# Performance work log

Hardware: AMD Instinct MI355X
Metric: run time of the kernel (lower is better)

Reference implementation:

```python
import jax, jax.numpy as jnp
import numpy as np

N_AGENT = 25
N_S = 32
N_A = 4
HID = 128
EHH_HID = HID * N_AGENT          # 3200
INTER = 150                      # INTERMEDIATE_NODES
BATCH = 2048
N_EDGE = 300


def _leaky(x):
    return jnp.where(x >= 0, x, 0.01 * x)


def setup_inputs() -> dict:
    key = jax.random.key(0)
    ks = jax.random.split(key, 12)
    states = jax.random.normal(ks[0], (N_AGENT, BATCH, N_S), dtype=jnp.float32)
    ehh_w = jax.random.normal(ks[1], (N_AGENT * N_S, EHH_HID), dtype=jnp.float32) * 0.05
    anova = jax.random.normal(ks[2], (EHH_HID + INTER, N_AGENT), dtype=jnp.float32)
    w1 = jax.random.normal(ks[3], (N_AGENT, EHH_HID, 12), dtype=jnp.float32) * 0.02
    b1 = jax.random.normal(ks[4], (N_AGENT, 12), dtype=jnp.float32) * 0.02
    w2 = jax.random.normal(ks[5], (N_AGENT, 12, 12), dtype=jnp.float32) * 0.3
    b2 = jax.random.normal(ks[6], (N_AGENT, 12), dtype=jnp.float32) * 0.02
    w3 = jax.random.normal(ks[7], (N_AGENT, 12, N_A), dtype=jnp.float32) * 0.3
    b3 = jax.random.normal(ks[8], (N_AGENT, N_A), dtype=jnp.float32) * 0.02
    actions = jax.random.randint(ks[9], (N_AGENT, BATCH), 0, N_A, dtype=jnp.int32)
    # adjacency rows: (bi_att_row, neighbor_row_a, unused, neighbor_row_b)
    c0 = jax.random.randint(ks[10], (N_EDGE, 1), 0, INTER, dtype=jnp.int32)
    c13 = jax.random.randint(ks[11], (N_EDGE, 2), 0, EHH_HID, dtype=jnp.int32)
    adj = jnp.concatenate([c0, c13[:, :1], jnp.zeros((N_EDGE, 1), jnp.int32), c13[:, 1:]], axis=1)
    return {"states": states, "ehh_w": ehh_w, "anova": anova,
            "w1": w1, "b1": b1, "w2": w2, "b2": b2, "w3": w3, "b3": b3,
            "actions": actions, "adj": adj}


def reference(states, ehh_w, anova, w1, b1, w2, b2, w3, b3, actions, adj):
    # states: (A, B, S) -> ehh_s: (B, A*S)   (torch.cat(states, dim=1))
    B = states.shape[1]
    ehh_s = jnp.transpose(states, (1, 0, 2)).reshape(B, -1)
    # EHH normalization (BatchNorm, affine=False, batch stats) + linear + LeakyReLU
    mu = jnp.mean(ehh_s, axis=0, keepdims=True)
    var = jnp.var(ehh_s, axis=0, keepdims=True)
    ehh_n = (ehh_s - mu) * jax.lax.rsqrt(var + 1e-5)
    ehh_embedding = _leaky(ehh_n @ ehh_w)                    # (B, EHH_HID)

    # ANOVA attention assembly via adjacency scatter
    self_att = anova[:EHH_HID, :]                            # (EHH_HID, A)
    bi_att = anova[EHH_HID:, :]                              # (INTER, A)
    vals = bi_att[adj[:, 0], :]                              # (E, A)
    neighbor_att = jnp.zeros((EHH_HID, N_AGENT), jnp.float32)
    neighbor_att = neighbor_att.at[adj[:, 1]].set(vals)
    neighbor_att = neighbor_att.at[adj[:, 3]].set(vals)
    all_att = (self_att + neighbor_att).T                    # (A, EHH_HID)

    # att_s repeat/permute/reshape == broadcast of embedding per agent
    att_out = ehh_embedding[:, None, :] * all_att[None, :, :]  # (B, A, EHH_HID)

    # per-agent critics (ehh_hidden -> 12 -> 12 -> n_a)
    h1 = _leaky(jnp.einsum('bah,ahk->bak', att_out, w1) + b1[None])
    h2 = _leaky(jnp.einsum('bak,akj->baj', h1, w2) + b2[None])
    all_q = jnp.einsum('baj,ajc->bac', h2, w3) + b3[None]     # (B, A, N_A)

    # q = all_q.gather(1, in_acs) per agent -> (A, B)
    q = jnp.take_along_axis(all_q, actions.T[:, :, None], axis=2)[..., 0].T
    return q
```

## Files before the change

kernel.cpp:

```cpp
#include <hip/hip_runtime.h>
#include <cstdint>

#define NAG 25
#define NS 32
#define EHH 3200
#define KDIM 800
#define BATCH 2048
#define NEDGE 300
#define NPAD 384
#define KSPLIT 5

typedef _Float16 half8 __attribute__((ext_vector_type(8)));
typedef float f32x4 __attribute__((ext_vector_type(4)));

__device__ __forceinline__ float leaky(float x) { return x >= 0.f ? x : 0.01f * x; }

__global__ __launch_bounds__(256)
void prep1_kernel(const float* __restrict__ states, const float* __restrict__ ehh_w,
                  const int* __restrict__ adj, const float* __restrict__ anova,
                  const float* __restrict__ w1,
                  float* __restrict__ mean, float* __restrict__ rstd,
                  _Float16* __restrict__ wt, _Float16* __restrict__ w2dt) {
    __shared__ float redS[32][32];
    __shared__ float redQ[32][32];
    __shared__ float tile[32][33];
    __shared__ int win[EHH];
    const int bi = blockIdx.x;
    const int tid = threadIdx.x;

    if (bi < 25) {
        const int a = bi;
        const int s4 = (tid & 7) << 2;
        const int r0 = tid >> 3;
        const float* base = states + ((size_t)a * BATCH + r0) * NS + s4;
        f32x4 sum = {0.f, 0.f, 0.f, 0.f};
        f32x4 sq  = {0.f, 0.f, 0.f, 0.f};
#pragma unroll 8
        for (int it = 0; it < 64; ++it) {
            f32x4 v = *(const f32x4*)(base + (size_t)it * 32 * NS);
            sum += v;
            sq  += v * v;
        }
        *(f32x4*)&redS[r0][s4] = sum;
        *(f32x4*)&redQ[r0][s4] = sq;
        __syncthreads();
        if (tid < 32) {
            float s = 0.f, q = 0.f;
#pragma unroll
            for (int r = 0; r < 32; ++r) { s += redS[r][tid]; q += redQ[r][tid]; }
            float m = s * (1.f / BATCH);
            float var = q * (1.f / BATCH) - m * m;
            mean[a * 32 + tid] = m;
            rstd[a * 32 + tid] = rsqrtf(var + 1e-5f);
        }
    } else if (bi < 2525) {
        const int bb = bi - 25;
        const int n0 = (bb % 100) * 32, k0 = (bb / 100) * 32;
        const int x = tid & 31, y = tid >> 5;
        for (int i = y; i < 32; i += 8)
            tile[i][x] = ehh_w[(size_t)(k0 + i) * EHH + n0 + x];
        __syncthreads();
        for (int i = y; i < 32; i += 8)
            wt[(size_t)(n0 + i) * KDIM + k0 + x] = (_Float16)tile[x][i];
    } else {
        const int bb = bi - 2525;
        if (bb < 313) {
            for (int h = tid; h < EHH; h += 256) win[h] = -1;
            __syncthreads();
            for (int e = tid; e < 2 * NEDGE; e += 256) {
                int pass = e >= NEDGE;
                int ee = pass ? e - NEDGE : e;
                int dest = adj[ee * 4 + (pass ? 3 : 1)];
                atomicMax(&win[dest], e);
            }
            __syncthreads();
            int t = bb * 256 + tid;
            if (t < NAG * EHH) {
                int a = t / EHH;
                int h = t - a * EHH;
                float att = anova[(size_t)h * NAG + a];
                int w = win[h];
                if (w >= 0) {
                    int ee = w >= NEDGE ? w - NEDGE : w;
                    att += anova[(size_t)(EHH + adj[ee * 4]) * NAG + a];
                }
                const float* wp = w1 + ((size_t)a * EHH + h) * 12;
#pragma unroll
                for (int kk = 0; kk < 12; ++kk)
                    w2dt[(size_t)(a * 12 + kk) * EHH + h] = (_Float16)(att * wp[kk]);
            }
        } else {
            int p = (bb - 313) * 256 + tid;
            if (p < (NPAD - 300) * EHH / 8) {
                half8 z = {0, 0, 0, 0, 0, 0, 0, 0};
                ((half8*)(w2dt + (size_t)300 * EHH))[p] = z;
            }
        }
    }
}

__global__ __launch_bounds__(256)
void norm_kernel(const float* __restrict__ states, const float* __restrict__ mean,
                 const float* __restrict__ rstd, _Float16* __restrict__ A) {
    int u = blockIdx.x * 256 + threadIdx.x;
    int b = u / 100;
    int fo = (u - b * 100) * 8;
    int a = fo >> 5, s = fo & 31;
    const float* sp = states + ((size_t)a * BATCH + b) * NS + s;
    f32x4 v0 = *(const f32x4*)sp;
    f32x4 v1 = *(const f32x4*)(sp + 4);
    f32x4 m0 = *(const f32x4*)(mean + fo);
    f32x4 m1 = *(const f32x4*)(mean + fo + 4);
    f32x4 r0 = *(const f32x4*)(rstd + fo);
    f32x4 r1 = *(const f32x4*)(rstd + fo + 4);
    half8 out;
#pragma unroll
    for (int i = 0; i < 4; ++i) out[i] = (_Float16)((v0[i] - m0[i]) * r0[i]);
#pragma unroll
    for (int i = 0; i < 4; ++i) out[4 + i] = (_Float16)((v1[i] - m1[i]) * r1[i]);
    *(half8*)(A + (size_t)b * KDIM + fo) = out;
}

__device__ __forceinline__ void async16(const void* g, void* l) {
    __builtin_amdgcn_global_load_lds(
        (const __attribute__((address_space(1))) void*)(uintptr_t)g,
        (__attribute__((address_space(3))) void*)(unsigned)(uintptr_t)l, 16, 0, 0);
}

template <int MI, int NI, bool LEAKY_F16_OUT>
__global__ __launch_bounds__(256)
void gemm_bt(const _Float16* __restrict__ A, const _Float16* __restrict__ B,
             _Float16* __restrict__ Ch, float* __restrict__ Cf,
             int Ktot, int ldc, int kPerSplit, int slabStride) {
    constexpr int BM = MI * 32;
    constexpr int BN = NI * 32;
    __shared__ __attribute__((aligned(16))) _Float16 As[2][BM * 32];
    __shared__ __attribute__((aligned(16))) _Float16 Bs[2][BN * 32];
    const int tid = threadIdx.x;
    const int lane = tid & 63;
    const int wave = tid >> 6;
    const int wm = (wave >> 1) * (MI * 16);
    const int wn = (wave & 1) * (NI * 16);

    const int gx = gridDim.x, gy = gridDim.y;
    int nwg = gx * gy * gridDim.z;
    int bidf = blockIdx.x + gx * (blockIdx.y + gy * blockIdx.z);
    int swz = (bidf & 7) * (nwg >> 3) + (bidf >> 3);
    const int bx = swz % gx;
    const int rem = swz / gx;
    const int by = rem % gy;
    const int bz = rem / gy;

    const int m0 = bx * BM;
    const int n0 = by * BN;
    const int k0 = bz * kPerSplit;
    const int nk = kPerSplit >> 5;

    const int srow = lane >> 2;
    const int scol = (lane & 3) << 3;
    const _Float16* gA0 = A + (size_t)(m0 + wave * 16 + srow) * Ktot + k0 + scol;
    const _Float16* gA1 = gA0 + (size_t)64 * Ktot;
    const _Float16* gB0 = B + (size_t)(n0 + wave * 16 + srow) * Ktot + k0 + scol;
    const _Float16* gB1 = gB0 + (size_t)64 * Ktot;
    const int lofs = wave * 512;

    f32x4 acc[MI][NI];
    const f32x4 zero = {0.f, 0.f, 0.f, 0.f};
#pragma unroll
    for (int i = 0; i < MI; ++i)
#pragma unroll
        for (int j = 0; j < NI; ++j) acc[i][j] = zero;

    const int fr = lane & 15;
    const int q8 = (lane >> 4) << 3;

    async16(gA0, As[0] + lofs);
    if constexpr (BM == 128) async16(gA1, As[0] + 2048 + lofs);
    async16(gB0, Bs[0] + lofs);
    if constexpr (BN == 128) async16(gB1, Bs[0] + 2048 + lofs);

    for (int kt = 0; kt < nk; ++kt) {
        const int cur = kt & 1;
        __syncthreads();
        if (kt + 1 < nk) {
            const int ko = (kt + 1) << 5;
            const int nxt = cur ^ 1;
            async16(gA0 + ko, As[nxt] + lofs);
            if constexpr (BM == 128) async16(gA1 + ko, As[nxt] + 2048 + lofs);
            async16(gB0 + ko, Bs[nxt] + lofs);
            if constexpr (BN == 128) async16(gB1 + ko, Bs[nxt] + 2048 + lofs);
        }
        half8 av[MI], bv[NI];
#pragma unroll
        for (int i = 0; i < MI; ++i)
            av[i] = *(const half8*)(As[cur] + (wm + i * 16 + fr) * 32 + q8);
#pragma unroll
        for (int j = 0; j < NI; ++j)
            bv[j] = *(const half8*)(Bs[cur] + (wn + j * 16 + fr) * 32 + q8);
#pragma unroll
        for (int i = 0; i < MI; ++i)
#pragma unroll
            for (int j = 0; j < NI; ++j)
                acc[i][j] = __builtin_amdgcn_mfma_f32_16x16x32_f16(av[i], bv[j], acc[i][j], 0, 0, 0);
    }

    const int r0 = (lane >> 4) << 2;
    if (LEAKY_F16_OUT) {
#pragma unroll
        for (int i = 0; i < MI; ++i)
#pragma unroll
            for (int j = 0; j < NI; ++j)
#pragma unroll
                for (int r = 0; r < 4; ++r) {
                    int row = m0 + wm + i * 16 + r0 + r;
                    int col = n0 + wn + j * 16 + fr;
                    Ch[(size_t)row * ldc + col] = (_Float16)leaky(acc[i][j][r]);
                }
    } else {
        float* C = Cf + (size_t)bz * slabStride;
#pragma unroll
        for (int i = 0; i < MI; ++i)
#pragma unroll
            for (int j = 0; j < NI; ++j)
#pragma unroll
                for (int r = 0; r < 4; ++r) {
                    int row = m0 + wm + i * 16 + r0 + r;
                    int col = n0 + wn + j * 16 + fr;
                    C[(size_t)row * ldc + col] = acc[i][j][r];
                }
    }
}

__global__ void tail_kernel(const float* __restrict__ Hp, const float* __restrict__ b1,
                            const float* __restrict__ w2, const float* __restrict__ b2,
                            const float* __restrict__ w3, const float* __restrict__ b3,
                            const int* __restrict__ act, float* __restrict__ out) {
    int t = blockIdx.x * 256 + threadIdx.x;
    int b = t & (BATCH - 1);
    int a = t >> 11;
    const float* hp = Hp + (size_t)b * NPAD + a * 12;
    float h1[12];
#pragma unroll
    for (int k = 0; k < 12; ++k) {
        float s = b1[a * 12 + k];
#pragma unroll
        for (int ks = 0; ks < KSPLIT; ++ks) s += hp[(size_t)ks * BATCH * NPAD + k];
        h1[k] = leaky(s);
    }
    float h2[12];
#pragma unroll
    for (int j = 0; j < 12; ++j) {
        float s = b2[a * 12 + j];
#pragma unroll
        for (int k = 0; k < 12; ++k) s += h1[k] * w2[(a * 12 + k) * 12 + j];
        h2[j] = leaky(s);
    }
    int c = act[t];
    float q = b3[a * 4 + c];
#pragma unroll
    for (int j = 0; j < 12; ++j) q += h2[j] * w3[(a * 12 + j) * 4 + c];
    out[t] = q;
}

extern "C" void kernel_launch(void* const* d_in, const int* in_sizes, int n_in,
                              void* d_out, int out_size, void* d_ws, size_t ws_size,
                              hipStream_t stream) {
    (void)in_sizes; (void)n_in; (void)out_size; (void)ws_size;
    const float* states = (const float*)d_in[0];
    const float* ehh_w  = (const float*)d_in[1];
    const float* anova  = (const float*)d_in[2];
    const float* w1     = (const float*)d_in[3];
    const float* b1     = (const float*)d_in[4];
    const float* w2     = (const float*)d_in[5];
    const float* b2     = (const float*)d_in[6];
    const float* w3     = (const float*)d_in[7];
    const float* b3     = (const float*)d_in[8];
    const int* actions  = (const int*)d_in[9];
    const int* adj      = (const int*)d_in[10];
    float* out = (float*)d_out;

    char* ws = (char*)d_ws;
    float*     mean   = (float*)    (ws + 0);
    float*     rstd   = (float*)    (ws + 4096);
    _Float16*  Abf    = (_Float16*) (ws + 32768);
    _Float16*  WbT    = (_Float16*) (ws + 3311616);
    _Float16*  W2dT   = (_Float16*) (ws + 8433664);
    _Float16*  emb    = (_Float16*) (ws + 10893312);
    float*     Hp     = (float*)    (ws + 24002560);

    prep1_kernel<<<2970, 256, 0, stream>>>(states, ehh_w, adj, anova, w1,
                                           mean, rstd, WbT, W2dT);
    norm_kernel<<<800, 256, 0, stream>>>(states, mean, rstd, Abf);
    gemm_bt<4, 2, true><<<dim3(16, 50, 1), 256, 0, stream>>>(Abf, WbT, emb, nullptr,
                                                             KDIM, EHH, KDIM, 0);
    gemm_bt<2, 4, false><<<dim3(32, 3, KSPLIT), 256, 0, stream>>>(emb, W2dT, nullptr, Hp,
                                                                  EHH, NPAD, EHH / KSPLIT,
                                                                  BATCH * NPAD);
    tail_kernel<<<(BATCH * NAG) / 256, 256, 0, stream>>>(Hp, b1, w2, b2, w3, b3, actions, out);
}
```

Baseline: 135.4 us.

## Fuse all stages into one cooperative persistent kernel with grid syncs

Replaces the five separate launches with a single cooperative kernel of 800 blocks that runs prep, normalization, both GEMMs and the tail in sequence, separated by grid-wide barriers. Each stage is refactored into a device function sharing one static shared-memory buffer. The aim is to remove per-launch overhead and inter-kernel gaps. In exchange, work is confined to a fixed grid (prep loops over virtual blocks, later stages idle many blocks) and grid.sync adds barrier cost. A fallback to the old multi-kernel path is kept for when the cooperative launch fails.

```diff
diff --git a/kernel.cpp b/kernel.cpp
--- a/kernel.cpp
+++ b/kernel.cpp
@@ -1,5 +1,8 @@
 #include <hip/hip_runtime.h>
+#include <hip/hip_cooperative_groups.h>
 #include <cstdint>
+
+namespace cg = cooperative_groups;
 
 #define NAG 25
 #define NS 32
@@ -9,27 +12,29 @@
 #define NEDGE 300
 #define NPAD 384
 #define KSPLIT 5
+#define NB 800
 
 typedef _Float16 half8 __attribute__((ext_vector_type(8)));
 typedef float f32x4 __attribute__((ext_vector_type(4)));
 
 __device__ __forceinline__ float leaky(float x) { return x >= 0.f ? x : 0.01f * x; }
 
-__global__ __launch_bounds__(256)
-void prep1_kernel(const float* __restrict__ states, const float* __restrict__ ehh_w,
-                  const int* __restrict__ adj, const float* __restrict__ anova,
-                  const float* __restrict__ w1,
-                  float* __restrict__ mean, float* __restrict__ rstd,
-                  _Float16* __restrict__ wt, _Float16* __restrict__ w2dt) {
-    __shared__ float redS[32][32];
-    __shared__ float redQ[32][32];
-    __shared__ float tile[32][33];
-    __shared__ int win[EHH];
-    const int bi = blockIdx.x;
-    const int tid = threadIdx.x;
-
-    if (bi < 25) {
-        const int a = bi;
+__device__ __forceinline__ void async16(const void* g, void* l) {
+    __builtin_amdgcn_global_load_lds(
+        (const __attribute__((address_space(1))) void*)(uintptr_t)g,
+        (__attribute__((address_space(3))) void*)(unsigned)(uintptr_t)l, 16, 0, 0);
+}
+
+
+__device__ __forceinline__ void prep_role(char* smem, int vb, int tid,
+        const float* __restrict__ states, const float* __restrict__ ehh_w,
+        const int* __restrict__ adj, const float* __restrict__ anova,
+        const float* __restrict__ w1, float* __restrict__ mean, float* __restrict__ rstd,
+        _Float16* __restrict__ wt, _Float16* __restrict__ w2dt) {
+    if (vb < 25) {
+        float* redS = (float*)smem;
+        float* redQ = redS + 1024;
+        const int a = vb;
         const int s4 = (tid & 7) << 2;
         const int r0 = tid >> 3;
         const float* base = states + ((size_t)a * BATCH + r0) * NS + s4;
@@ -41,20 +46,21 @@
             sum += v;
             sq  += v * v;
         }
-        *(f32x4*)&redS[r0][s4] = sum;
-        *(f32x4*)&redQ[r0][s4] = sq;
+        *(f32x4*)&redS[r0 * 32 + s4] = sum;
+        *(f32x4*)&redQ[r0 * 32 + s4] = sq;
         __syncthreads();
         if (tid < 32) {
             float s = 0.f, q = 0.f;
 #pragma unroll
-            for (int r = 0; r < 32; ++r) { s += redS[r][tid]; q += redQ[r][tid]; }
+            for (int r = 0; r < 32; ++r) { s += redS[r * 32 + tid]; q += redQ[r * 32 + tid]; }
             float m = s * (1.f / BATCH);
             float var = q * (1.f / BATCH) - m * m;
             mean[a * 32 + tid] = m;
             rstd[a * 32 + tid] = rsqrtf(var + 1e-5f);
         }
-    } else if (bi < 2525) {
-        const int bb = bi - 25;
+    } else if (vb < 2525) {
+        float (*tile)[33] = (float(*)[33])smem;
+        const int bb = vb - 25;
         const int n0 = (bb % 100) * 32, k0 = (bb / 100) * 32;
         const int x = tid & 31, y = tid >> 5;
         for (int i = y; i < 32; i += 8)
@@ -63,8 +69,9 @@
         for (int i = y; i < 32; i += 8)
             wt[(size_t)(n0 + i) * KDIM + k0 + x] = (_Float16)tile[x][i];
     } else {
-        const int bb = bi - 2525;
+        const int bb = vb - 2525;
         if (bb < 313) {
+            int* win = (int*)smem;
             for (int h = tid; h < EHH; h += 256) win[h] = -1;
             __syncthreads();
             for (int e = tid; e < 2 * NEDGE; e += 256) {
@@ -99,10 +106,9 @@
     }
 }
 
-__global__ __launch_bounds__(256)
-void norm_kernel(const float* __restrict__ states, const float* __restrict__ mean,
-                 const float* __restrict__ rstd, _Float16* __restrict__ A) {
-    int u = blockIdx.x * 256 + threadIdx.x;
+__device__ __forceinline__ void norm_role(int u,
+        const float* __restrict__ states, const float* __restrict__ mean,
+        const float* __restrict__ rstd, _Float16* __restrict__ A) {
     int b = u / 100;
     int fo = (u - b * 100) * 8;
     int a = fo >> 5, s = fo & 31;
@@ -113,39 +119,31 @@
     f32x4 m1 = *(const f32x4*)(mean + fo + 4);
     f32x4 r0 = *(const f32x4*)(rstd + fo);
     f32x4 r1 = *(const f32x4*)(rstd + fo + 4);
-    half8 out;
-#pragma unroll
-    for (int i = 0; i < 4; ++i) out[i] = (_Float16)((v0[i] - m0[i]) * r0[i]);
-#pragma unroll
-    for (int i = 0; i < 4; ++i) out[4 + i] = (_Float16)((v1[i] - m1[i]) * r1[i]);
-    *(half8*)(A + (size_t)b * KDIM + fo) = out;
-}
-
-__device__ __forceinline__ void async16(const void* g, void* l) {
-    __builtin_amdgcn_global_load_lds(
-        (const __attribute__((address_space(1))) void*)(uintptr_t)g,
-        (__attribute__((address_space(3))) void*)(unsigned)(uintptr_t)l, 16, 0, 0);
+    half8 o;
+#pragma unroll
+    for (int i = 0; i < 4; ++i) o[i] = (_Float16)((v0[i] - m0[i]) * r0[i]);
+#pragma unroll
+    for (int i = 0; i < 4; ++i) o[4 + i] = (_Float16)((v1[i] - m1[i]) * r1[i]);
+    *(half8*)(A + (size_t)b * KDIM + fo) = o;
 }
 
 template <int MI, int NI, bool LEAKY_F16_OUT>
-__global__ __launch_bounds__(256)
-void gemm_bt(const _Float16* __restrict__ A, const _Float16* __restrict__ B,
-             _Float16* __restrict__ Ch, float* __restrict__ Cf,
-             int Ktot, int ldc, int kPerSplit, int slabStride) {
+__device__ __forceinline__ void gemm_stage(char* smem, int tile,
+        const _Float16* __restrict__ A, const _Float16* __restrict__ B,
+        _Float16* __restrict__ Ch, float* __restrict__ Cf,
+        int Ktot, int ldc, int kPerSplit, int slabStride, int gx, int gy, int gz) {
     constexpr int BM = MI * 32;
     constexpr int BN = NI * 32;
-    __shared__ __attribute__((aligned(16))) _Float16 As[2][BM * 32];
-    __shared__ __attribute__((aligned(16))) _Float16 Bs[2][BN * 32];
+    _Float16* As = (_Float16*)smem;
+    _Float16* Bs = (_Float16*)(smem + 4 * BM * 32);
     const int tid = threadIdx.x;
     const int lane = tid & 63;
     const int wave = tid >> 6;
     const int wm = (wave >> 1) * (MI * 16);
     const int wn = (wave & 1) * (NI * 16);
 
-    const int gx = gridDim.x, gy = gridDim.y;
-    int nwg = gx * gy * gridDim.z;
-    int bidf = blockIdx.x + gx * (blockIdx.y + gy * blockIdx.z);
-    int swz = (bidf & 7) * (nwg >> 3) + (bidf >> 3);
+    const int nwg = gx * gy * gz;
+    int swz = (tile & 7) * (nwg >> 3) + (tile >> 3);
     const int bx = swz % gx;
     const int rem = swz / gx;
     const int by = rem % gy;
@@ -174,10 +172,10 @@
     const int fr = lane & 15;
     const int q8 = (lane >> 4) << 3;
 
-    async16(gA0, As[0] + lofs);
-    if constexpr (BM == 128) async16(gA1, As[0] + 2048 + lofs);
-    async16(gB0, Bs[0] + lofs);
-    if constexpr (BN == 128) async16(gB1, Bs[0] + 2048 + lofs);
+    async16(gA0, As + lofs);
+    if constexpr (BM == 128) async16(gA1, As + 2048 + lofs);
+    async16(gB0, Bs + lofs);
+    if constexpr (BN == 128) async16(gB1, Bs + 2048 + lofs);
 
     for (int kt = 0; kt < nk; ++kt) {
         const int cur = kt & 1;
@@ -185,18 +183,18 @@
         if (kt + 1 < nk) {
             const int ko = (kt + 1) << 5;
             const int nxt = cur ^ 1;
-            async16(gA0 + ko, As[nxt] + lofs);
-            if constexpr (BM == 128) async16(gA1 + ko, As[nxt] + 2048 + lofs);
-            async16(gB0 + ko, Bs[nxt] + lofs);
-            if constexpr (BN == 128) async16(gB1 + ko, Bs[nxt] + 2048 + lofs);
+            async16(gA0 + ko, As + nxt * (BM * 32) + lofs);
+            if constexpr (BM == 128) async16(gA1 + ko, As + nxt * (BM * 32) + 2048 + lofs);
+            async16(gB0 + ko, Bs + nxt * (BN * 32) + lofs);
+            if constexpr (BN == 128) async16(gB1 + ko, Bs + nxt * (BN * 32) + 2048 + lofs);
         }
         half8 av[MI], bv[NI];
 #pragma unroll
         for (int i = 0; i < MI; ++i)
-            av[i] = *(const half8*)(As[cur] + (wm + i * 16 + fr) * 32 + q8);
+            av[i] = *(const half8*)(As + cur * (BM * 32) + (wm + i * 16 + fr) * 32 + q8);
 #pragma unroll
         for (int j = 0; j < NI; ++j)
-            bv[j] = *(const half8*)(Bs[cur] + (wn + j * 16 + fr) * 32 + q8);
+            bv[j] = *(const half8*)(Bs + cur * (BN * 32) + (wn + j * 16 + fr) * 32 + q8);
 #pragma unroll
         for (int i = 0; i < MI; ++i)
 #pragma unroll
@@ -231,35 +229,102 @@
     }
 }
 
+__device__ __forceinline__ void tail_role(int t,
+        const float* __restrict__ Hp, const float* __restrict__ b1,
+        const float* __restrict__ w2, const float* __restrict__ b2,
+        const float* __restrict__ w3, const float* __restrict__ b3,
+        const int* __restrict__ act, float* __restrict__ out) {
+    int b = t & (BATCH - 1);
+    int a = t >> 11;
+    const float* hp = Hp + (size_t)b * NPAD + a * 12;
+    float h1[12];
+#pragma unroll
+    for (int k = 0; k < 12; ++k) {
+        float s = b1[a * 12 + k];
+#pragma unroll
+        for (int ks = 0; ks < KSPLIT; ++ks) s += hp[(size_t)ks * BATCH * NPAD + k];
+        h1[k] = leaky(s);
+    }
+    float h2[12];
+#pragma unroll
+    for (int j = 0; j < 12; ++j) {
+        float s = b2[a * 12 + j];
+#pragma unroll
+        for (int k = 0; k < 12; ++k) s += h1[k] * w2[(a * 12 + k) * 12 + j];
+        h2[j] = leaky(s);
+    }
+    int c = act[t];
+    float q = b3[a * 4 + c];
+#pragma unroll
+    for (int j = 0; j < 12; ++j) q += h2[j] * w3[(a * 12 + j) * 4 + c];
+    out[t] = q;
+}
+
+__global__ __launch_bounds__(256, 4)
+void mega_kernel(const float* __restrict__ states, const float* __restrict__ ehh_w,
+                 const float* __restrict__ anova, const float* __restrict__ w1,
+                 const float* __restrict__ b1, const float* __restrict__ w2,
+                 const float* __restrict__ b2, const float* __restrict__ w3,
+                 const float* __restrict__ b3, const int* __restrict__ actions,
+                 const int* __restrict__ adj, float* __restrict__ out,
+                 float* __restrict__ mean, float* __restrict__ rstd,
+                 _Float16* __restrict__ Abf, _Float16* __restrict__ WbT,
+                 _Float16* __restrict__ W2dT, _Float16* __restrict__ emb,
+                 float* __restrict__ Hp) {
+    cg::grid_group grid = cg::this_grid();
+    __shared__ __attribute__((aligned(16))) char smem[24576];
+    const int tid = threadIdx.x;
+    const int bid = blockIdx.x;
+
+    for (int vb = bid; vb < 2970; vb += NB) {
+        prep_role(smem, vb, tid, states, ehh_w, adj, anova, w1, mean, rstd, WbT, W2dT);
+        __syncthreads();
+    }
+    grid.sync();
+    norm_role(bid * 256 + tid, states, mean, rstd, Abf);
+    grid.sync();
+    gemm_stage<4, 2, true>(smem, bid, Abf, WbT, emb, nullptr, KDIM, EHH, KDIM, 0, 16, 50, 1);
+    grid.sync();
+    if (bid < 480)
+        gemm_stage<2, 4, false>(smem, bid, emb, W2dT, nullptr, Hp, EHH, NPAD,
+                                EHH / KSPLIT, BATCH * NPAD, 32, 3, KSPLIT);
+    grid.sync();
+    if (bid < 200)
+        tail_role(bid * 256 + tid, Hp, b1, w2, b2, w3, b3, actions, out);
+}
+
+__global__ __launch_bounds__(256)
+void prep1_kernel(const float* __restrict__ states, const float* __restrict__ ehh_w,
+                  const int* __restrict__ adj, const float* __restrict__ anova,
+                  const float* __restrict__ w1,
+                  float* __restrict__ mean, float* __restrict__ rstd,
+                  _Float16* __restrict__ wt, _Float16* __restrict__ w2dt) {
+    __shared__ __attribute__((aligned(16))) char smem[24576];
+    prep_role(smem, blockIdx.x, threadIdx.x, states, ehh_w, adj, anova, w1, mean, rstd, wt, w2dt);
+}
+
+__global__ __launch_bounds__(256)
+void norm_kernel(const float* __restrict__ states, const float* __restrict__ mean,
+                 const float* __restrict__ rstd, _Float16* __restrict__ A) {
+    norm_role(blockIdx.x * 256 + threadIdx.x, states, mean, rstd, A);
+}
+
+template <int MI, int NI, bool LEAKY_F16_OUT>
+__global__ __launch_bounds__(256)
+void gemm_bt(const _Float16* __restrict__ A, const _Float16* __restrict__ B,
+             _Float16* __restrict__ Ch, float* __restrict__ Cf,
+             int Ktot, int ldc, int kPerSplit, int slabStride, int gx, int gy, int gz) {
+    __shared__ __attribute__((aligned(16))) char smem[24576];
+    int tile = blockIdx.x + gx * (blockIdx.y + gy * blockIdx.z);
+    gemm_stage<MI, NI, LEAKY_F16_OUT>(smem, tile, A, B, Ch, Cf, Ktot, ldc, kPerSplit,
+                                      slabStride, gx, gy, gz);
+}
+
 __global__ void tail_kernel(const float* __restrict__ Hp, const float* __restrict__ b1,
                             const float* __restrict__ w2, const float* __restrict__ b2,
                             const float* __restrict__ w3, const float* __restrict__ b3,
                             const int* __restrict__ act, float* __restrict__ out) {
-    int t = blockIdx.x * 256 + threadIdx.x;
-    int b = t & (BATCH - 1);
-    int a = t >> 11;
-    const float* hp = Hp + (size_t)b * NPAD + a * 12;
-    float h1[12];
-#pragma unroll
-    for (int k = 0; k < 12; ++k) {
-        float s = b1[a * 12 + k];
-#pragma unroll
-        for (int ks = 0; ks < KSPLIT; ++ks) s += hp[(size_t)ks * BATCH * NPAD + k];
-        h1[k] = leaky(s);
-    }
-    float h2[12];
-#pragma unroll
-    for (int j = 0; j < 12; ++j) {
-        float s = b2[a * 12 + j];
-#pragma unroll
-        for (int k = 0; k < 12; ++k) s += h1[k] * w2[(a * 12 + k) * 12 + j];
-        h2[j] = leaky(s);
-    }
-    int c = act[t];
-    float q = b3[a * 4 + c];
-#pragma unroll
-    for (int j = 0; j < 12; ++j) q += h2[j] * w3[(a * 12 + j) * 4 + c];
-    out[t] = q;
+    tail_role(blockIdx.x * 256 + threadIdx.x, Hp, b1, w2, b2, w3, b3, act, out);
 }
 
 extern "C" void kernel_launch(void* const* d_in, const int* in_sizes, int n_in,
@@ -288,13 +353,23 @@
     _Float16*  emb    = (_Float16*) (ws + 10893312);
     float*     Hp     = (float*)    (ws + 24002560);
 
-    prep1_kernel<<<2970, 256, 0, stream>>>(states, ehh_w, adj, anova, w1,
-                                           mean, rstd, WbT, W2dT);
-    norm_kernel<<<800, 256, 0, stream>>>(states, mean, rstd, Abf);
-    gemm_bt<4, 2, true><<<dim3(16, 50, 1), 256, 0, stream>>>(Abf, WbT, emb, nullptr,
-                                                             KDIM, EHH, KDIM, 0);
-    gemm_bt<2, 4, false><<<dim3(32, 3, KSPLIT), 256, 0, stream>>>(emb, W2dT, nullptr, Hp,
-                                                                  EHH, NPAD, EHH / KSPLIT,
-                                                                  BATCH * NPAD);
-    tail_kernel<<<(BATCH * NAG) / 256, 256, 0, stream>>>(Hp, b1, w2, b2, w3, b3, actions, out);
-}
+    void* args[] = {
+        (void*)&states, (void*)&ehh_w, (void*)&anova, (void*)&w1, (void*)&b1,
+        (void*)&w2, (void*)&b2, (void*)&w3, (void*)&b3, (void*)&actions, (void*)&adj,
+        (void*)&out, (void*)&mean, (void*)&rstd, (void*)&Abf, (void*)&WbT,
+        (void*)&W2dT, (void*)&emb, (void*)&Hp
+    };
+    hipError_t err = hipLaunchCooperativeKernel((const void*)mega_kernel, dim3(NB),
+                                                dim3(256), args, 0, stream);
+    if (err != hipSuccess) {
+        prep1_kernel<<<2970, 256, 0, stream>>>(states, ehh_w, adj, anova, w1,
+                                               mean, rstd, WbT, W2dT);
+        norm_kernel<<<800, 256, 0, stream>>>(states, mean, rstd, Abf);
+        gemm_bt<4, 2, true><<<dim3(16, 50, 1), 256, 0, stream>>>(Abf, WbT, emb, nullptr,
+                                                                 KDIM, EHH, KDIM, 0, 16, 50, 1);
+        gemm_bt<2, 4, false><<<dim3(32, 3, KSPLIT), 256, 0, stream>>>(emb, W2dT, nullptr, Hp,
+                                                                      EHH, NPAD, EHH / KSPLIT,
+                                                                      BATCH * NPAD, 32, 3, KSPLIT);
+        tail_kernel<<<(BATCH * NAG) / 256, 256, 0, stream>>>(Hp, b1, w2, b2, w3, b3, actions, out);
+    }
+}
```

Measured after the change: 533.3 us. 294% more time.

## Fuse batch-norm normalization into first GEMM's A-tile load and co-schedule W2 prep

Applied to the files above, without the earlier changes.

Removes the separate normalization kernel and its fp16 intermediate. The first GEMM now reads fp32 states directly, normalizes with the mean and rstd vectors and writes fp16 A tiles into LDS in a register-prefetched pipeline. The attention-weighted W2 preparation blocks move from the prep kernel into the same launch as GEMM1, run as extra blocks. This cuts one launch and a global round trip. The cost is a synchronous register-staged A path instead of async LDS loads, and mixed block roles in one grid.

```diff
diff --git a/kernel.cpp b/kernel.cpp
--- a/kernel.cpp
+++ b/kernel.cpp
@@ -15,16 +15,19 @@
 
 __device__ __forceinline__ float leaky(float x) { return x >= 0.f ? x : 0.01f * x; }
 
+__device__ __forceinline__ void async16(const void* g, void* l) {
+    __builtin_amdgcn_global_load_lds(
+        (const __attribute__((address_space(1))) void*)(uintptr_t)g,
+        (__attribute__((address_space(3))) void*)(unsigned)(uintptr_t)l, 16, 0, 0);
+}
+
 __global__ __launch_bounds__(256)
 void prep1_kernel(const float* __restrict__ states, const float* __restrict__ ehh_w,
-                  const int* __restrict__ adj, const float* __restrict__ anova,
-                  const float* __restrict__ w1,
                   float* __restrict__ mean, float* __restrict__ rstd,
-                  _Float16* __restrict__ wt, _Float16* __restrict__ w2dt) {
+                  _Float16* __restrict__ wt) {
     __shared__ float redS[32][32];
     __shared__ float redQ[32][32];
     __shared__ float tile[32][33];
-    __shared__ int win[EHH];
     const int bi = blockIdx.x;
     const int tid = threadIdx.x;
 
@@ -53,7 +56,7 @@
             mean[a * 32 + tid] = m;
             rstd[a * 32 + tid] = rsqrtf(var + 1e-5f);
         }
-    } else if (bi < 2525) {
+    } else {
         const int bb = bi - 25;
         const int n0 = (bb % 100) * 32, k0 = (bb / 100) * 32;
         const int x = tid & 31, y = tid >> 5;
@@ -62,9 +65,22 @@
         __syncthreads();
         for (int i = y; i < 32; i += 8)
             wt[(size_t)(n0 + i) * KDIM + k0 + x] = (_Float16)tile[x][i];
-    } else {
-        const int bb = bi - 2525;
+    }
+}
+
+__global__ __launch_bounds__(256)
+void gemm1_kernel(const float* __restrict__ states, const _Float16* __restrict__ B,
+                  const float* __restrict__ mean, const float* __restrict__ rstd,
+                  const float* __restrict__ anova, const int* __restrict__ adj,
+                  const float* __restrict__ w1,
+                  _Float16* __restrict__ emb, _Float16* __restrict__ w2dt) {
+    __shared__ __attribute__((aligned(16))) char smem[24576];
+    const int tid = threadIdx.x;
+
+    if (blockIdx.x >= 800) {
+        const int bb = blockIdx.x - 800;
         if (bb < 313) {
+            int* win = (int*)smem;
             for (int h = tid; h < EHH; h += 256) win[h] = -1;
             __syncthreads();
             for (int e = tid; e < 2 * NEDGE; e += 256) {
@@ -96,42 +112,128 @@
                 ((half8*)(w2dt + (size_t)300 * EHH))[p] = z;
             }
         }
-    }
-}
-
-__global__ __launch_bounds__(256)
-void norm_kernel(const float* __restrict__ states, const float* __restrict__ mean,
-                 const float* __restrict__ rstd, _Float16* __restrict__ A) {
-    int u = blockIdx.x * 256 + threadIdx.x;
-    int b = u / 100;
-    int fo = (u - b * 100) * 8;
-    int a = fo >> 5, s = fo & 31;
-    const float* sp = states + ((size_t)a * BATCH + b) * NS + s;
-    f32x4 v0 = *(const f32x4*)sp;
-    f32x4 v1 = *(const f32x4*)(sp + 4);
-    f32x4 m0 = *(const f32x4*)(mean + fo);
-    f32x4 m1 = *(const f32x4*)(mean + fo + 4);
-    f32x4 r0 = *(const f32x4*)(rstd + fo);
-    f32x4 r1 = *(const f32x4*)(rstd + fo + 4);
-    half8 out;
-#pragma unroll
-    for (int i = 0; i < 4; ++i) out[i] = (_Float16)((v0[i] - m0[i]) * r0[i]);
-#pragma unroll
-    for (int i = 0; i < 4; ++i) out[4 + i] = (_Float16)((v1[i] - m1[i]) * r1[i]);
-    *(half8*)(A + (size_t)b * KDIM + fo) = out;
-}
-
-__device__ __forceinline__ void async16(const void* g, void* l) {
-    __builtin_amdgcn_global_load_lds(
-        (const __attribute__((address_space(1))) void*)(uintptr_t)g,
-        (__attribute__((address_space(3))) void*)(unsigned)(uintptr_t)l, 16, 0, 0);
-}
-
-template <int MI, int NI, bool LEAKY_F16_OUT>
+        return;
+    }
+
+    _Float16* As = (_Float16*)smem;
+    _Float16* Bs = (_Float16*)(smem + 16384);
+    const int lane = tid & 63;
+    const int wave = tid >> 6;
+    const int wm = (wave >> 1) * 64;
+    const int wn = (wave & 1) * 32;
+
+    int swz = (blockIdx.x & 7) * 100 + (blockIdx.x >> 3);
+    const int bx = swz & 15;
+    const int by = swz >> 4;
+    const int m0 = bx << 7;
+    const int n0 = by << 6;
+    const int nk = KDIM / 32;
+
+    const int arow = wave * 16 + (lane >> 2);
+    const int akk = (lane & 3) << 3;
+    const float* gA = states + ((size_t)m0 + arow) * NS + akk;
+    const int ldsA = wave * 1024 + lane * 16;
+
+    const int srow = lane >> 2;
+    const int scol = (lane & 3) << 3;
+    const _Float16* gB0 = B + (size_t)(n0 + wave * 16 + srow) * KDIM + scol;
+    const int lofsB = wave * 512;
+
+    f32x4 acc[4][2];
+    const f32x4 zero = {0.f, 0.f, 0.f, 0.f};
+#pragma unroll
+    for (int i = 0; i < 4; ++i)
+#pragma unroll
+        for (int j = 0; j < 2; ++j) acc[i][j] = zero;
+
+    const int fr = lane & 15;
+    const int q8 = (lane >> 4) << 3;
+
+    {
+        f32x4 a0 = *(const f32x4*)gA;
+        f32x4 a1 = *(const f32x4*)(gA + 4);
+        f32x4 a2 = *(const f32x4*)(gA + (size_t)64 * NS);
+        f32x4 a3 = *(const f32x4*)(gA + (size_t)64 * NS + 4);
+        f32x4 mv0 = *(const f32x4*)(mean + akk);
+        f32x4 mv1 = *(const f32x4*)(mean + akk + 4);
+        f32x4 rv0 = *(const f32x4*)(rstd + akk);
+        f32x4 rv1 = *(const f32x4*)(rstd + akk + 4);
+        half8 o0, o1;
+#pragma unroll
+        for (int i = 0; i < 4; ++i) {
+            o0[i]     = (_Float16)((a0[i] - mv0[i]) * rv0[i]);
+            o0[4 + i] = (_Float16)((a1[i] - mv1[i]) * rv1[i]);
+            o1[i]     = (_Float16)((a2[i] - mv0[i]) * rv0[i]);
+            o1[4 + i] = (_Float16)((a3[i] - mv1[i]) * rv1[i]);
+        }
+        *(half8*)((char*)As + ldsA) = o0;
+        *(half8*)((char*)As + 4096 + ldsA) = o1;
+        async16(gB0, Bs + lofsB);
+    }
+
+    for (int kt = 0; kt < nk; ++kt) {
+        const int cur = kt & 1;
+        const int nxt = cur ^ 1;
+        __syncthreads();
+        f32x4 a0, a1, a2, a3, mv0, mv1, rv0, rv1;
+        const bool more = (kt + 1 < nk);
+        if (more) {
+            async16(gB0 + (kt + 1) * 32, Bs + nxt * 2048 + lofsB);
+            const float* gAn = gA + (size_t)(kt + 1) * BATCH * NS;
+            a0 = *(const f32x4*)gAn;
+            a1 = *(const f32x4*)(gAn + 4);
+            a2 = *(const f32x4*)(gAn + (size_t)64 * NS);
+            a3 = *(const f32x4*)(gAn + (size_t)64 * NS + 4);
+            const float* mp = mean + (kt + 1) * 32 + akk;
+            const float* rp = rstd + (kt + 1) * 32 + akk;
+            mv0 = *(const f32x4*)mp;
+            mv1 = *(const f32x4*)(mp + 4);
+            rv0 = *(const f32x4*)rp;
+            rv1 = *(const f32x4*)(rp + 4);
+        }
+        half8 av[4], bv[2];
+#pragma unroll
+        for (int i = 0; i < 4; ++i)
+            av[i] = *(const half8*)(As + cur * 4096 + (wm + i * 16 + fr) * 32 + q8);
+#pragma unroll
+        for (int j = 0; j < 2; ++j)
+            bv[j] = *(const half8*)(Bs + cur * 2048 + (wn + j * 16 + fr) * 32 + q8);
+#pragma unroll
+        for (int i = 0; i < 4; ++i)
+#pragma unroll
+            for (int j = 0; j < 2; ++j)
+                acc[i][j] = __builtin_amdgcn_mfma_f32_16x16x32_f16(av[i], bv[j], acc[i][j], 0, 0, 0);
+        if (more) {
+            half8 o0, o1;
+#pragma unroll
+            for (int i = 0; i < 4; ++i) {
+                o0[i]     = (_Float16)((a0[i] - mv0[i]) * rv0[i]);
+                o0[4 + i] = (_Float16)((a1[i] - mv1[i]) * rv1[i]);
+                o1[i]     = (_Float16)((a2[i] - mv0[i]) * rv0[i]);
+                o1[4 + i] = (_Float16)((a3[i] - mv1[i]) * rv1[i]);
+            }
+            *(half8*)((char*)As + nxt * 8192 + ldsA) = o0;
+            *(half8*)((char*)As + nxt * 8192 + 4096 + ldsA) = o1;
+        }
+    }
+
+    const int r0 = (lane >> 4) << 2;
+#pragma unroll
+    for (int i = 0; i < 4; ++i)
+#pragma unroll
+        for (int j = 0; j < 2; ++j)
+#pragma unroll
+            for (int r = 0; r < 4; ++r) {
+                int row = m0 + wm + i * 16 + r0 + r;
+                int col = n0 + wn + j * 16 + fr;
+                emb[(size_t)row * EHH + col] = (_Float16)leaky(acc[i][j][r]);
+            }
+}
+
+template <int MI, int NI>
 __global__ __launch_bounds__(256)
 void gemm_bt(const _Float16* __restrict__ A, const _Float16* __restrict__ B,
-             _Float16* __restrict__ Ch, float* __restrict__ Cf,
-             int Ktot, int ldc, int kPerSplit, int slabStride) {
+             float* __restrict__ Cf, int Ktot, int ldc, int kPerSplit, int slabStride) {
     constexpr int BM = MI * 32;
     constexpr int BN = NI * 32;
     __shared__ __attribute__((aligned(16))) _Float16 As[2][BM * 32];
@@ -159,7 +261,6 @@
     const int srow = lane >> 2;
     const int scol = (lane & 3) << 3;
     const _Float16* gA0 = A + (size_t)(m0 + wave * 16 + srow) * Ktot + k0 + scol;
-    const _Float16* gA1 = gA0 + (size_t)64 * Ktot;
     const _Float16* gB0 = B + (size_t)(n0 + wave * 16 + srow) * Ktot + k0 + scol;
     const _Float16* gB1 = gB0 + (size_t)64 * Ktot;
     const int lofs = wave * 512;
@@ -175,7 +276,6 @@
     const int q8 = (lane >> 4) << 3;
 
     async16(gA0, As[0] + lofs);
-    if constexpr (BM == 128) async16(gA1, As[0] + 2048 + lofs);
     async16(gB0, Bs[0] + lofs);
     if constexpr (BN == 128) async16(gB1, Bs[0] + 2048 + lofs);
 
@@ -186,7 +286,6 @@
             const int ko = (kt + 1) << 5;
             const int nxt = cur ^ 1;
             async16(gA0 + ko, As[nxt] + lofs);
-            if constexpr (BM == 128) async16(gA1 + ko, As[nxt] + 2048 + lofs);
             async16(gB0 + ko, Bs[nxt] + lofs);
             if constexpr (BN == 128) async16(gB1 + ko, Bs[nxt] + 2048 + lofs);
         }
@@ -205,30 +304,17 @@
     }
 
     const int r0 = (lane >> 4) << 2;
-    if (LEAKY_F16_OUT) {
-#pragma unroll
-        for (int i = 0; i < MI; ++i)
-#pragma unroll
-            for (int j = 0; j < NI; ++j)
-#pragma unroll
-                for (int r = 0; r < 4; ++r) {
-                    int row = m0 + wm + i * 16 + r0 + r;
-                    int col = n0 + wn + j * 16 + fr;
-                    Ch[(size_t)row * ldc + col] = (_Float16)leaky(acc[i][j][r]);
-                }
-    } else {
-        float* C = Cf + (size_t)bz * slabStride;
-#pragma unroll
-        for (int i = 0; i < MI; ++i)
-#pragma unroll
-            for (int j = 0; j < NI; ++j)
-#pragma unroll
-                for (int r = 0; r < 4; ++r) {
-                    int row = m0 + wm + i * 16 + r0 + r;
-                    int col = n0 + wn + j * 16 + fr;
-                    C[(size_t)row * ldc + col] = acc[i][j][r];
-                }
-    }
+    float* C = Cf + (size_t)bz * slabStride;
+#pragma unroll
+    for (int i = 0; i < MI; ++i)
+#pragma unroll
+        for (int j = 0; j < NI; ++j)
+#pragma unroll
+            for (int r = 0; r < 4; ++r) {
+                int row = m0 + wm + i * 16 + r0 + r;
+                int col = n0 + wn + j * 16 + fr;
+                C[(size_t)row * ldc + col] = acc[i][j][r];
+            }
 }
 
 __global__ void tail_kernel(const float* __restrict__ Hp, const float* __restrict__ b1,
@@ -282,19 +368,16 @@
     char* ws = (char*)d_ws;
     float*     mean   = (float*)    (ws + 0);
     float*     rstd   = (float*)    (ws + 4096);
-    _Float16*  Abf    = (_Float16*) (ws + 32768);
     _Float16*  WbT    = (_Float16*) (ws + 3311616);
     _Float16*  W2dT   = (_Float16*) (ws + 8433664);
     _Float16*  emb    = (_Float16*) (ws + 10893312);
     float*     Hp     = (float*)    (ws + 24002560);
 
-    prep1_kernel<<<2970, 256, 0, stream>>>(states, ehh_w, adj, anova, w1,
-                                           mean, rstd, WbT, W2dT);
-    norm_kernel<<<800, 256, 0, stream>>>(states, mean, rstd, Abf);
-    gemm_bt<4, 2, true><<<dim3(16, 50, 1), 256, 0, stream>>>(Abf, WbT, emb, nullptr,
-                                                             KDIM, EHH, KDIM, 0);
-    gemm_bt<2, 4, false><<<dim3(32, 3, KSPLIT), 256, 0, stream>>>(emb, W2dT, nullptr, Hp,
-                                                                  EHH, NPAD, EHH / KSPLIT,
-                                                                  BATCH * NPAD);
+    prep1_kernel<<<2525, 256, 0, stream>>>(states, ehh_w, mean, rstd, WbT);
+    gemm1_kernel<<<1245, 256, 0, stream>>>(states, WbT, mean, rstd, anova, adj, w1,
+                                           emb, W2dT);
+    gemm_bt<2, 4><<<dim3(32, 3, KSPLIT), 256, 0, stream>>>(emb, W2dT, Hp,
+                                                           EHH, NPAD, EHH / KSPLIT,
+                                                           BATCH * NPAD);
     tail_kernel<<<(BATCH * NAG) / 256, 256, 0, stream>>>(Hp, b1, w2, b2, w3, b3, actions, out);
 }
```

Result: slower. 150.6 us (+11.2%).

## Fuse split-K tail into second GEMM via last-block counter; merge norm into prep

Applied to the files above, without the earlier changes.

Splits the old prep kernel into a tiny stats kernel and a larger independent kernel that also performs the normalization, so the norm kernel launch disappears and its work runs alongside the weight transposes. The second GEMM now counts finished split-K blocks per row tile with an atomic counter, and the last block for that tile does the split-K reduction and per-agent MLP tail in place, removing the separate tail launch. This trades launch overhead for serialized tail work inside 32 last-arriving blocks and a reliance on threadfence/atomic ordering.

```diff
diff --git a/kernel.cpp b/kernel.cpp
--- a/kernel.cpp
+++ b/kernel.cpp
@@ -15,46 +15,81 @@
 
 __device__ __forceinline__ float leaky(float x) { return x >= 0.f ? x : 0.01f * x; }
 
+__device__ __forceinline__ void async16(const void* g, void* l) {
+    __builtin_amdgcn_global_load_lds(
+        (const __attribute__((address_space(1))) void*)(uintptr_t)g,
+        (__attribute__((address_space(3))) void*)(unsigned)(uintptr_t)l, 16, 0, 0);
+}
+
 __global__ __launch_bounds__(256)
-void prep1_kernel(const float* __restrict__ states, const float* __restrict__ ehh_w,
-                  const int* __restrict__ adj, const float* __restrict__ anova,
-                  const float* __restrict__ w1,
-                  float* __restrict__ mean, float* __restrict__ rstd,
-                  _Float16* __restrict__ wt, _Float16* __restrict__ w2dt) {
+void stats_kernel(const float* __restrict__ states, float* __restrict__ mean,
+                  float* __restrict__ rstd, int* __restrict__ cnt) {
     __shared__ float redS[32][32];
     __shared__ float redQ[32][32];
+    const int bi = blockIdx.x;
+    const int tid = threadIdx.x;
+    if (bi == 25) {
+        if (tid < 32) cnt[tid] = 0;
+        return;
+    }
+    const int a = bi;
+    const int s4 = (tid & 7) << 2;
+    const int r0 = tid >> 3;
+    const float* base = states + ((size_t)a * BATCH + r0) * NS + s4;
+    f32x4 sum = {0.f, 0.f, 0.f, 0.f};
+    f32x4 sq  = {0.f, 0.f, 0.f, 0.f};
+#pragma unroll 8
+    for (int it = 0; it < 64; ++it) {
+        f32x4 v = *(const f32x4*)(base + (size_t)it * 32 * NS);
+        sum += v;
+        sq  += v * v;
+    }
+    *(f32x4*)&redS[r0][s4] = sum;
+    *(f32x4*)&redQ[r0][s4] = sq;
+    __syncthreads();
+    if (tid < 32) {
+        float s = 0.f, q = 0.f;
+#pragma unroll
+        for (int r = 0; r < 32; ++r) { s += redS[r][tid]; q += redQ[r][tid]; }
+        float m = s * (1.f / BATCH);
+        float var = q * (1.f / BATCH) - m * m;
+        mean[a * 32 + tid] = m;
+        rstd[a * 32 + tid] = rsqrtf(var + 1e-5f);
+    }
+}
+
+__global__ __launch_bounds__(256)
+void indep_kernel(const float* __restrict__ states, const float* __restrict__ ehh_w,
+                  const float* __restrict__ mean, const float* __restrict__ rstd,
+                  const float* __restrict__ anova, const int* __restrict__ adj,
+                  const float* __restrict__ w1,
+                  _Float16* __restrict__ A, _Float16* __restrict__ wt,
+                  _Float16* __restrict__ w2dt) {
     __shared__ float tile[32][33];
     __shared__ int win[EHH];
     const int bi = blockIdx.x;
     const int tid = threadIdx.x;
 
-    if (bi < 25) {
-        const int a = bi;
-        const int s4 = (tid & 7) << 2;
-        const int r0 = tid >> 3;
-        const float* base = states + ((size_t)a * BATCH + r0) * NS + s4;
-        f32x4 sum = {0.f, 0.f, 0.f, 0.f};
-        f32x4 sq  = {0.f, 0.f, 0.f, 0.f};
-#pragma unroll 8
-        for (int it = 0; it < 64; ++it) {
-            f32x4 v = *(const f32x4*)(base + (size_t)it * 32 * NS);
-            sum += v;
-            sq  += v * v;
-        }
-        *(f32x4*)&redS[r0][s4] = sum;
-        *(f32x4*)&redQ[r0][s4] = sq;
-        __syncthreads();
-        if (tid < 32) {
-            float s = 0.f, q = 0.f;
-#pragma unroll
-            for (int r = 0; r < 32; ++r) { s += redS[r][tid]; q += redQ[r][tid]; }
-            float m = s * (1.f / BATCH);
-            float var = q * (1.f / BATCH) - m * m;
-            mean[a * 32 + tid] = m;
-            rstd[a * 32 + tid] = rsqrtf(var + 1e-5f);
-        }
-    } else if (bi < 2525) {
-        const int bb = bi - 25;
+    if (bi < 800) {
+        int u = bi * 256 + tid;
+        int b = u / 100;
+        int fo = (u - b * 100) * 8;
+        int a = fo >> 5, s = fo & 31;
+        const float* sp = states + ((size_t)a * BATCH + b) * NS + s;
+        f32x4 v0 = *(const f32x4*)sp;
+        f32x4 v1 = *(const f32x4*)(sp + 4);
+        f32x4 m0 = *(const f32x4*)(mean + fo);
+        f32x4 m1 = *(const f32x4*)(mean + fo + 4);
+        f32x4 r0 = *(const f32x4*)(rstd + fo);
+        f32x4 r1 = *(const f32x4*)(rstd + fo + 4);
+        half8 o;
+#pragma unroll
+        for (int i = 0; i < 4; ++i) o[i] = (_Float16)((v0[i] - m0[i]) * r0[i]);
+#pragma unroll
+        for (int i = 0; i < 4; ++i) o[4 + i] = (_Float16)((v1[i] - m1[i]) * r1[i]);
+        *(half8*)(A + (size_t)b * KDIM + fo) = o;
+    } else if (bi < 3300) {
+        const int bb = bi - 800;
         const int n0 = (bb % 100) * 32, k0 = (bb / 100) * 32;
         const int x = tid & 31, y = tid >> 5;
         for (int i = y; i < 32; i += 8)
@@ -63,7 +98,7 @@
         for (int i = y; i < 32; i += 8)
             wt[(size_t)(n0 + i) * KDIM + k0 + x] = (_Float16)tile[x][i];
     } else {
-        const int bb = bi - 2525;
+        const int bb = bi - 3300;
         if (bb < 313) {
             for (int h = tid; h < EHH; h += 256) win[h] = -1;
             __syncthreads();
@@ -99,39 +134,10 @@
     }
 }
 
-__global__ __launch_bounds__(256)
-void norm_kernel(const float* __restrict__ states, const float* __restrict__ mean,
-                 const float* __restrict__ rstd, _Float16* __restrict__ A) {
-    int u = blockIdx.x * 256 + threadIdx.x;
-    int b = u / 100;
-    int fo = (u - b * 100) * 8;
-    int a = fo >> 5, s = fo & 31;
-    const float* sp = states + ((size_t)a * BATCH + b) * NS + s;
-    f32x4 v0 = *(const f32x4*)sp;
-    f32x4 v1 = *(const f32x4*)(sp + 4);
-    f32x4 m0 = *(const f32x4*)(mean + fo);
-    f32x4 m1 = *(const f32x4*)(mean + fo + 4);
-    f32x4 r0 = *(const f32x4*)(rstd + fo);
-    f32x4 r1 = *(const f32x4*)(rstd + fo + 4);
-    half8 out;
-#pragma unroll
-    for (int i = 0; i < 4; ++i) out[i] = (_Float16)((v0[i] - m0[i]) * r0[i]);
-#pragma unroll
-    for (int i = 0; i < 4; ++i) out[4 + i] = (_Float16)((v1[i] - m1[i]) * r1[i]);
-    *(half8*)(A + (size_t)b * KDIM + fo) = out;
-}
-
-__device__ __forceinline__ void async16(const void* g, void* l) {
-    __builtin_amdgcn_global_load_lds(
-        (const __attribute__((address_space(1))) void*)(uintptr_t)g,
-        (__attribute__((address_space(3))) void*)(unsigned)(uintptr_t)l, 16, 0, 0);
-}
-
-template <int MI, int NI, bool LEAKY_F16_OUT>
+template <int MI, int NI>
 __global__ __launch_bounds__(256)
 void gemm_bt(const _Float16* __restrict__ A, const _Float16* __restrict__ B,
-             _Float16* __restrict__ Ch, float* __restrict__ Cf,
-             int Ktot, int ldc, int kPerSplit, int slabStride) {
+             _Float16* __restrict__ Ch, int Ktot, int ldc, int kPerSplit) {
     constexpr int BM = MI * 32;
     constexpr int BN = NI * 32;
     __shared__ __attribute__((aligned(16))) _Float16 As[2][BM * 32];
@@ -161,7 +167,6 @@
     const _Float16* gA0 = A + (size_t)(m0 + wave * 16 + srow) * Ktot + k0 + scol;
     const _Float16* gA1 = gA0 + (size_t)64 * Ktot;
     const _Float16* gB0 = B + (size_t)(n0 + wave * 16 + srow) * Ktot + k0 + scol;
-    const _Float16* gB1 = gB0 + (size_t)64 * Ktot;
     const int lofs = wave * 512;
 
     f32x4 acc[MI][NI];
@@ -177,7 +182,6 @@
     async16(gA0, As[0] + lofs);
     if constexpr (BM == 128) async16(gA1, As[0] + 2048 + lofs);
     async16(gB0, Bs[0] + lofs);
-    if constexpr (BN == 128) async16(gB1, Bs[0] + 2048 + lofs);
 
     for (int kt = 0; kt < nk; ++kt) {
         const int cur = kt & 1;
@@ -188,7 +192,6 @@
             async16(gA0 + ko, As[nxt] + lofs);
             if constexpr (BM == 128) async16(gA1 + ko, As[nxt] + 2048 + lofs);
             async16(gB0 + ko, Bs[nxt] + lofs);
-            if constexpr (BN == 128) async16(gB1 + ko, Bs[nxt] + 2048 + lofs);
         }
         half8 av[MI], bv[NI];
 #pragma unroll
@@ -205,61 +208,143 @@
     }
 
     const int r0 = (lane >> 4) << 2;
-    if (LEAKY_F16_OUT) {
+#pragma unroll
+    for (int i = 0; i < MI; ++i)
+#pragma unroll
+        for (int j = 0; j < NI; ++j)
+#pragma unroll
+            for (int r = 0; r < 4; ++r) {
+                int row = m0 + wm + i * 16 + r0 + r;
+                int col = n0 + wn + j * 16 + fr;
+                Ch[(size_t)row * ldc + col] = (_Float16)leaky(acc[i][j][r]);
+            }
+}
+
+__global__ __launch_bounds__(256)
+void gemm2_tail(const _Float16* __restrict__ A, const _Float16* __restrict__ B,
+                float* __restrict__ Hp, int* __restrict__ cnt,
+                const float* __restrict__ b1, const float* __restrict__ w2,
+                const float* __restrict__ b2, const float* __restrict__ w3,
+                const float* __restrict__ b3, const int* __restrict__ act,
+                float* __restrict__ out) {
+    constexpr int MI = 2, NI = 4, BM = 64, BN = 128;
+    constexpr int Ktot = EHH, kPerSplit = EHH / KSPLIT;
+    __shared__ __attribute__((aligned(16))) _Float16 As[2][BM * 32];
+    __shared__ __attribute__((aligned(16))) _Float16 Bs[2][BN * 32];
+    __shared__ int lastFlag;
+    const int tid = threadIdx.x;
+    const int lane = tid & 63;
+    const int wave = tid >> 6;
+    const int wm = (wave >> 1) * (MI * 16);
+    const int wn = (wave & 1) * (NI * 16);
+
+    int bidf = blockIdx.x + 32 * (blockIdx.y + 3 * blockIdx.z);
+    int swz = (bidf & 7) * 60 + (bidf >> 3);
+    const int bx = swz % 32;
+    const int rem = swz / 32;
+    const int by = rem % 3;
+    const int bz = rem / 3;
+
+    const int m0 = bx * BM;
+    const int n0 = by * BN;
+    const int k0 = bz * kPerSplit;
+    const int nk = kPerSplit >> 5;
+
+    const int srow = lane >> 2;
+    const int scol = (lane & 3) << 3;
+    const _Float16* gA0 = A + (size_t)(m0 + wave * 16 + srow) * Ktot + k0 + scol;
+    const _Float16* gB0 = B + (size_t)(n0 + wave * 16 + srow) * Ktot + k0 + scol;
+    const _Float16* gB1 = gB0 + (size_t)64 * Ktot;
+    const int lofs = wave * 512;
+
+    f32x4 acc[MI][NI];
+    const f32x4 zero = {0.f, 0.f, 0.f, 0.f};
+#pragma unroll
+    for (int i = 0; i < MI; ++i)
+#pragma unroll
+        for (int j = 0; j < NI; ++j) acc[i][j] = zero;
+
+    const int fr = lane & 15;
+    const int q8 = (lane >> 4) << 3;
+
+    async16(gA0, As[0] + lofs);
+    async16(gB0, Bs[0] + lofs);
+    async16(gB1, Bs[0] + 2048 + lofs);
+
+    for (int kt = 0; kt < nk; ++kt) {
+        const int cur = kt & 1;
+        __syncthreads();
+        if (kt + 1 < nk) {
+            const int ko = (kt + 1) << 5;
+            const int nxt = cur ^ 1;
+            async16(gA0 + ko, As[nxt] + lofs);
+            async16(gB0 + ko, Bs[nxt] + lofs);
+            async16(gB1 + ko, Bs[nxt] + 2048 + lofs);
+        }
+        half8 av[MI], bv[NI];
 #pragma unroll
         for (int i = 0; i < MI; ++i)
+            av[i] = *(const half8*)(As[cur] + (wm + i * 16 + fr) * 32 + q8);
+#pragma unroll
+        for (int j = 0; j < NI; ++j)
+            bv[j] = *(const half8*)(Bs[cur] + (wn + j * 16 + fr) * 32 + q8);
+#pragma unroll
+        for (int i = 0; i < MI; ++i)
 #pragma unroll
             for (int j = 0; j < NI; ++j)
-#pragma unroll
-                for (int r = 0; r < 4; ++r) {
-                    int row = m0 + wm + i * 16 + r0 + r;
-                    int col = n0 + wn + j * 16 + fr;
-                    Ch[(size_t)row * ldc + col] = (_Float16)leaky(acc[i][j][r]);
-                }
-    } else {
-        float* C = Cf + (size_t)bz * slabStride;
-#pragma unroll
-        for (int i = 0; i < MI; ++i)
-#pragma unroll
-            for (int j = 0; j < NI; ++j)
-#pragma unroll
-                for (int r = 0; r < 4; ++r) {
-                    int row = m0 + wm + i * 16 + r0 + r;
-                    int col = n0 + wn + j * 16 + fr;
-                    C[(size_t)row * ldc + col] = acc[i][j][r];
-                }
-    }
-}
-
-__global__ void tail_kernel(const float* __restrict__ Hp, const float* __restrict__ b1,
-                            const float* __restrict__ w2, const float* __restrict__ b2,
-                            const float* __restrict__ w3, const float* __restrict__ b3,
-                            const int* __restrict__ act, float* __restrict__ out) {
-    int t = blockIdx.x * 256 + threadIdx.x;
-    int b = t & (BATCH - 1);
-    int a = t >> 11;
-    const float* hp = Hp + (size_t)b * NPAD + a * 12;
-    float h1[12];
-#pragma unroll
-    for (int k = 0; k < 12; ++k) {
-        float s = b1[a * 12 + k];
-#pragma unroll
-        for (int ks = 0; ks < KSPLIT; ++ks) s += hp[(size_t)ks * BATCH * NPAD + k];
-        h1[k] = leaky(s);
-    }
-    float h2[12];
-#pragma unroll
-    for (int j = 0; j < 12; ++j) {
-        float s = b2[a * 12 + j];
-#pragma unroll
-        for (int k = 0; k < 12; ++k) s += h1[k] * w2[(a * 12 + k) * 12 + j];
-        h2[j] = leaky(s);
-    }
-    int c = act[t];
-    float q = b3[a * 4 + c];
-#pragma unroll
-    for (int j = 0; j < 12; ++j) q += h2[j] * w3[(a * 12 + j) * 4 + c];
-    out[t] = q;
+                acc[i][j] = __builtin_amdgcn_mfma_f32_16x16x32_f16(av[i], bv[j], acc[i][j], 0, 0, 0);
+    }
+
+    const int r0 = (lane >> 4) << 2;
+    float* C = Hp + (size_t)bz * (BATCH * NPAD);
+#pragma unroll
+    for (int i = 0; i < MI; ++i)
+#pragma unroll
+        for (int j = 0; j < NI; ++j)
+#pragma unroll
+            for (int r = 0; r < 4; ++r) {
+                int row = m0 + wm + i * 16 + r0 + r;
+                int col = n0 + wn + j * 16 + fr;
+                C[(size_t)row * NPAD + col] = acc[i][j][r];
+            }
+
+    __syncthreads();
+    if (tid == 0) {
+        __threadfence();
+        int old = atomicAdd(&cnt[bx], 1);
+        lastFlag = (old == 14);
+        if (old == 14) __threadfence();
+    }
+    __syncthreads();
+    if (!lastFlag) return;
+
+    for (int i = tid; i < 64 * NAG; i += 256) {
+        int rr = i & 63;
+        int a = i >> 6;
+        int row = m0 + rr;
+        const float* hp = Hp + (size_t)row * NPAD + a * 12;
+        float h1[12];
+#pragma unroll
+        for (int k = 0; k < 12; ++k) {
+            float s = b1[a * 12 + k];
+#pragma unroll
+            for (int ks = 0; ks < KSPLIT; ++ks) s += hp[(size_t)ks * BATCH * NPAD + k];
+            h1[k] = leaky(s);
+        }
+        float h2[12];
+#pragma unroll
+        for (int j = 0; j < 12; ++j) {
+            float s = b2[a * 12 + j];
+#pragma unroll
+            for (int k = 0; k < 12; ++k) s += h1[k] * w2[(a * 12 + k) * 12 + j];
+            h2[j] = leaky(s);
+        }
+        int c = act[a * BATCH + row];
+        float q = b3[a * 4 + c];
+#pragma unroll
+        for (int j = 0; j < 12; ++j) q += h2[j] * w3[(a * 12 + j) * 4 + c];
+        out[a * BATCH + row] = q;
+    }
 }
 
 extern "C" void kernel_launch(void* const* d_in, const int* in_sizes, int n_in,
@@ -282,19 +367,17 @@
     char* ws = (char*)d_ws;
     float*     mean   = (float*)    (ws + 0);
     float*     rstd   = (float*)    (ws + 4096);
+    int*       cnt    = (int*)      (ws + 8192);
     _Float16*  Abf    = (_Float16*) (ws + 32768);
     _Float16*  WbT    = (_Float16*) (ws + 3311616);
     _Float16*  W2dT   = (_Float16*) (ws + 8433664);
     _Float16*  emb    = (_Float16*) (ws + 10893312);
     float*     Hp     = (float*)    (ws + 24002560);
 
-    prep1_kernel<<<2970, 256, 0, stream>>>(states, ehh_w, adj, anova, w1,
-                                           mean, rstd, WbT, W2dT);
-    norm_kernel<<<800, 256, 0, stream>>>(states, mean, rstd, Abf);
-    gemm_bt<4, 2, true><<<dim3(16, 50, 1), 256, 0, stream>>>(Abf, WbT, emb, nullptr,
-                                                             KDIM, EHH, KDIM, 0);
-    gemm_bt<2, 4, false><<<dim3(32, 3, KSPLIT), 256, 0, stream>>>(emb, W2dT, nullptr, Hp,
-                                                                  EHH, NPAD, EHH / KSPLIT,
-                                                                  BATCH * NPAD);
-    tail_kernel<<<(BATCH * NAG) / 256, 256, 0, stream>>>(Hp, b1, w2, b2, w3, b3, actions, out);
-}
+    stats_kernel<<<26, 256, 0, stream>>>(states, mean, rstd, cnt);
+    indep_kernel<<<3745, 256, 0, stream>>>(states, ehh_w, mean, rstd, anova, adj, w1,
+                                           Abf, WbT, W2dT);
+    gemm_bt<4, 2><<<dim3(16, 50, 1), 256, 0, stream>>>(Abf, WbT, emb, KDIM, EHH, KDIM);
+    gemm2_tail<<<dim3(32, 3, KSPLIT), 256, 0, stream>>>(emb, W2dT, Hp, cnt,
+                                                        b1, w2, b2, w3, b3, actions, out);
+}
```

Measured after the change: 175.8 us. +29.8%, slower.
